# Kernel optimization log

Measured on AMD Instinct MI355X. Metric: run time of the kernel, lower is better.

The kernel has to match this reference:

```python
import jax, jax.numpy as jnp
import numpy as np

N_WIRES = 12
N_QLAYERS = 2
DIM = 2 ** N_WIRES


def setup_inputs() -> dict:
    key = jax.random.key(0)
    k0, k1, k2, k3 = jax.random.split(key, 4)
    x = jax.random.normal(k0, (2048, 1024), dtype=jnp.float32)
    # TT cores: ranks [1,16,1], input dims [32,32], output dims [8,9]
    core0 = jax.random.normal(k1, (1, 32, 8, 16), dtype=jnp.float32) * 0.05
    core1 = jax.random.normal(k2, (16, 32, 9, 1), dtype=jnp.float32) * 0.05
    tt_bias = jnp.zeros((72,), dtype=jnp.float32)
    global_angles = jax.random.normal(k3, (N_QLAYERS, N_WIRES, 3), dtype=jnp.float32) * 0.1
    return {"x": x, "core0": core0, "core1": core1, "tt_bias": tt_bias,
            "global_angles": global_angles}


def _rot(angles):
    # angles [..., 3] -> combined U = Rz @ Ry @ Rx, shape [..., 2, 2] complex64
    half = angles * 0.5
    cx, sx = jnp.cos(half[..., 0]), jnp.sin(half[..., 0])
    cy, sy = jnp.cos(half[..., 1]), jnp.sin(half[..., 1])
    cz, sz = jnp.cos(half[..., 2]), jnp.sin(half[..., 2])
    zero = jnp.zeros_like(cx)
    cplx = jax.lax.complex
    Rx = jnp.stack([jnp.stack([cplx(cx, zero), cplx(zero, -sx)], -1),
                    jnp.stack([cplx(zero, -sx), cplx(cx, zero)], -1)], -2)
    Ry = jnp.stack([jnp.stack([cplx(cy, zero), cplx(-sy, zero)], -1),
                    jnp.stack([cplx(sy, zero), cplx(cy, zero)], -1)], -2)
    ez, ezc = cplx(cz, -sz), cplx(cz, sz)  # exp(-i z/2), exp(+i z/2)
    zc = cplx(zero, zero)
    Rz = jnp.stack([jnp.stack([ez, zc], -1), jnp.stack([zc, ezc], -1)], -2)
    return jnp.einsum('...ij,...jk,...kl->...il', Rz, Ry, Rx)


def _apply_1q(state, U, w):
    # state [bsz, 2^n]; U [bsz, 2, 2]; wire 0 = most significant qubit
    bsz = state.shape[0]
    left, right = 2 ** w, 2 ** (N_WIRES - w - 1)
    s = state.reshape(bsz, left, 2, right)
    s = jnp.einsum('bij,bljr->blir', U, s)
    return s.reshape(bsz, DIM)


def _cnot(state, c, t):
    bsz = state.shape[0]
    s = state.reshape((bsz,) + (2,) * N_WIRES)
    s0 = jax.lax.index_in_dim(s, 0, c + 1, keepdims=True)
    s1 = jax.lax.index_in_dim(s, 1, c + 1, keepdims=True)
    s1 = jnp.flip(s1, axis=t + 1)  # flip target amplitudes where control = 1
    return jnp.concatenate([s0, s1], axis=c + 1).reshape(bsz, DIM)


def reference(x, core0, core1, tt_bias, global_angles):
    bsz = x.shape[0]
    # --- TT layer: x[b,32,32] contracted with two TT cores -> [b,8,9] -> [b,72]
    x_rs = x.reshape(bsz, 32, 32)
    tt_out = jnp.einsum('bij,aipq,qjrs->bpr', x_rs, core0, core1).reshape(bsz, -1) + tt_bias
    # residual global angles
    angles = global_angles[None, :, :, :] + tt_out.reshape(bsz, N_QLAYERS, N_WIRES, 3)
    U = _rot(angles)  # [bsz, L, n, 2, 2]
    # --- tensor-product Ry encoding of x[:, :n_wires] on |0...0>
    enc = x[:, :N_WIRES] * 0.5
    amp = jnp.stack([jnp.cos(enc), jnp.sin(enc)], -1)  # [bsz, n, 2]
    state = amp[:, 0, :]
    for w in range(1, N_WIRES):
        state = (state[:, :, None] * amp[:, w, None, :]).reshape(bsz, -1)
    state = state.astype(jnp.complex64)  # [bsz, 2^n]
    # --- VQC layers: fused Rz@Ry@Rx per wire, then ring CNOT (noise_prob=0)
    for k in range(N_QLAYERS):
        for w in range(N_WIRES):
            state = _apply_1q(state, U[:, k, w], w)
        for i in range(N_WIRES - 1):
            state = _cnot(state, i, i + 1)
        state = _cnot(state, N_WIRES - 1, 0)
    # --- MeasureAll(PauliZ): <Z_w> per wire
    probs = jnp.real(state * jnp.conj(state))  # [bsz, 2^n]
    idx = jnp.arange(DIM)[:, None]
    bits = (idx >> jnp.arange(N_WIRES - 1, -1, -1)[None, :]) & 1  # [2^n, n]
    zsign = (1.0 - 2.0 * bits).astype(jnp.float32)
    return probs @ zsign  # [bsz, n_wires]
```

## Files before the change

### kernel.cpp

```cpp
#include <hip/hip_runtime.h>
#include <math.h>

#define N_WIRES 12

__host__ __device__ constexpr int parity12(int x) {
  x ^= x >> 8; x ^= x >> 4; x ^= x >> 2; x ^= x >> 1;
  return x & 1;
}

__host__ __device__ constexpr int lanemask_of(int m) {
  return (((m >> 9) & 1) << 0) | (((m >> 8) & 1) << 1) |
         (((m >> 11) & 1) << 2) | (((m >> 10) & 1) << 3) |
         (((m >> 7) & 1) << 4) | (((m >> 6) & 1) << 5);
}

typedef float2 f2;
__device__ __forceinline__ f2 mk2(float a, float b) { f2 r; r.x = a; r.y = b; return r; }
__device__ __forceinline__ f2 pkmul(f2 a, f2 b) {
  f2 d; asm("v_pk_mul_f32 %0, %1, %2" : "=v"(d) : "v"(a), "v"(b)); return d;
}
__device__ __forceinline__ f2 pkfma(f2 a, f2 b, f2 c) {
  f2 d; asm("v_pk_fma_f32 %0, %1, %2, %3" : "=v"(d) : "v"(a), "v"(b), "v"(c)); return d;
}
__device__ __forceinline__ f2 swap2(f2 v) { return mk2(v.y, v.x); }

struct cpx { float r, i; };
__device__ __forceinline__ cpx cmulc(cpx a, cpx b) {
  return {a.r * b.r - a.i * b.i, a.r * b.i + a.i * b.r};
}
__device__ __forceinline__ cpx fpick(float r0, float i0, float r1, float i1, int b) {
  cpx c; c.r = b ? r1 : r0; c.i = b ? i1 : i0; return c;
}
__device__ __forceinline__ float rl(float v, int l) {
  return __int_as_float(__builtin_amdgcn_readlane(__float_as_int(v), l));
}

template <int LM>
__device__ __forceinline__ float lshfl(float v, int lane) {
  if constexpr (LM == 0) {
    return v;
  } else if constexpr (LM == 0x01) {
    return __int_as_float(__builtin_amdgcn_mov_dpp(__float_as_int(v), 0xB1, 0xF, 0xF, true));
  } else if constexpr (LM == 0x02) {
    return __int_as_float(__builtin_amdgcn_mov_dpp(__float_as_int(v), 0x4E, 0xF, 0xF, true));
  } else if constexpr (LM == 0x03) {
    return __int_as_float(__builtin_amdgcn_mov_dpp(__float_as_int(v), 0x1B, 0xF, 0xF, true));
  } else if constexpr ((LM & 0x20) != 0) {
#if __has_builtin(__builtin_amdgcn_permlane32_swap)
    auto p = __builtin_amdgcn_permlane32_swap(__float_as_int(v), __float_as_int(v), false, false);
    const float tv = __int_as_float((lane & 32) ? (int)p[0] : (int)p[1]);
    return lshfl<LM & 0x1F>(tv, lane);
#else
    return __shfl_xor(v, LM, 64);
#endif
  } else if constexpr (LM == 0x10) {
#if __has_builtin(__builtin_amdgcn_permlane16_swap)
    auto p = __builtin_amdgcn_permlane16_swap(__float_as_int(v), __float_as_int(v), false, false);
    return __int_as_float((lane & 16) ? (int)p[0] : (int)p[1]);
#else
    return __int_as_float(__builtin_amdgcn_ds_swizzle(__float_as_int(v), (0x10 << 10) | 0x1F));
#endif
  } else {
    return __int_as_float(__builtin_amdgcn_ds_swizzle(__float_as_int(v), (LM << 10) | 0x1F));
  }
}
template <int LM>
__device__ __forceinline__ f2 lshfl2(f2 v, int lane) {
  return mk2(lshfl<LM>(v.x, lane), lshfl<LM>(v.y, lane));
}

__global__ __launch_bounds__(256) void build_w_kernel(
    const float* __restrict__ core0,
    const float* __restrict__ core1,
    float* __restrict__ Wt) {
  int idx = blockIdx.x * 256 + threadIdx.x;
  int k = idx / 72;
  int o = idx - k * 72;
  int i = k >> 5, jj = k & 31;
  int p = o / 9, r = o - p * 9;
  float acc = 0.f;
#pragma unroll
  for (int q = 0; q < 16; ++q) {
    acc += core0[(i * 8 + p) * 16 + q] * core1[(q * 32 + jj) * 9 + r];
  }
  int og = o / 9, j = o - og * 9;
  Wt[k * 96 + og * 12 + j] = acc;
}

__global__ __launch_bounds__(512) void tt_gemm3(
    const float* __restrict__ x,
    const float* __restrict__ Wt,
    const float* __restrict__ bias,
    float* __restrict__ ttout) {
  __shared__ __align__(16) float xs[8 * 132];
  __shared__ float part[16 * 8 * 73];
  const int t = threadIdx.x;
  const int row0 = blockIdx.x * 8;
  const int kk = t >> 5;
  const int rp = (t >> 3) & 3;
  const int og = t & 7;
  const int r0 = rp * 2;

  float a0[9], a1[9];
#pragma unroll
  for (int j = 0; j < 9; ++j) { a0[j] = 0.f; a1[j] = 0.f; }

  for (int s = 0; s < 8; ++s) {
    __syncthreads();
    if (t < 256) {
      const int rr = t >> 5, j4 = t & 31;
      *(float4*)&xs[rr * 132 + j4 * 4] =
          *(const float4*)(x + (size_t)(row0 + rr) * 1024 + s * 128 + j4 * 4);
    }
    __syncthreads();
    const float* Wp = Wt + (size_t)s * 128 * 96;
#pragma unroll
    for (int i = 0; i < 8; ++i) {
      const int k = kk + i * 16;
      const float4 wA = *(const float4*)(Wp + k * 96 + og * 12);
      const float4 wB = *(const float4*)(Wp + k * 96 + og * 12 + 4);
      const float w8 = Wp[k * 96 + og * 12 + 8];
      const float x0v = xs[r0 * 132 + k];
      const float x1v = xs[r0 * 132 + 132 + k];
      a0[0] += x0v * wA.x; a0[1] += x0v * wA.y;
      a0[2] += x0v * wA.z; a0[3] += x0v * wA.w;
      a0[4] += x0v * wB.x; a0[5] += x0v * wB.y;
      a0[6] += x0v * wB.z; a0[7] += x0v * wB.w;
      a0[8] += x0v * w8;
      a1[0] += x1v * wA.x; a1[1] += x1v * wA.y;
      a1[2] += x1v * wA.z; a1[3] += x1v * wA.w;
      a1[4] += x1v * wB.x; a1[5] += x1v * wB.y;
      a1[6] += x1v * wB.z; a1[7] += x1v * wB.w;
      a1[8] += x1v * w8;
    }
  }

#pragma unroll
  for (int j = 0; j < 9; ++j) {
    part[(kk * 8 + r0) * 73 + og * 9 + j] = a0[j];
    part[(kk * 8 + r0 + 1) * 73 + og * 9 + j] = a1[j];
  }
  __syncthreads();

  for (int i = t; i < 576; i += 512) {
    const int r = i / 72, o = i - r * 72;
    float ssum = bias[o];
#pragma unroll
    for (int kq = 0; kq < 16; ++kq) ssum += part[(kq * 8 + r) * 73 + o];
    ttout[(size_t)(row0 + r) * 72 + o] = ssum;
  }
}

template <int MASK, int ROW>
__device__ __forceinline__ void gate_pk(f2 R[32], f2 I[32],
    float u00r, float u00i, float u01r, float u01i, int lane) {
  constexpr int RM = MASK & 0x3F;
  constexpr int LMP = lanemask_of(MASK);
  constexpr int ROWL = lanemask_of(ROW);
  constexpr int FLIP = parity12(ROW & 3);
  constexpr int JX = (RM == 0) ? 0 : (((RM & 1) ? (RM ^ 3) : RM) >> 1);
  constexpr bool SW = (RM & 1) != 0;

  const int tsgn = (__popc(ROWL & lane) & 1) << 31;
  const float dEi = __int_as_float(__float_as_int(u00i) ^ tsgn);
  const float oEr = __int_as_float(__float_as_int(u01r) ^ tsgn);
  const float ndEi = -dEi, noEr = -oEr;
  const f2 A  = mk2(u00r, u00r);
  const f2 C  = mk2(u01i, u01i);
  const f2 nC = mk2(-u01i, -u01i);

  auto Dof = [&](int pe, int ph) { return mk2(pe ? ndEi : dEi, ph ? ndEi : dEi); };
  auto Oof = [&](int pe, int ph) { return mk2(pe ? noEr : oEr, ph ? noEr : oEr); };

  auto upd = [&](int j, f2 Rb, f2 Ib, f2& outR, f2& outI) {
    const int pe = parity12(ROW & (2 * j));
    const int ph = pe ^ FLIP;
    const f2 Dj = Dof(pe, ph), nDj = Dof(!pe, !ph), Oj = Oof(pe, ph);
    const f2 a = R[j], ii = I[j];
    outR = pkfma(A, a, pkfma(nDj, ii, pkfma(Oj, Rb, pkmul(nC, Ib))));
    outI = pkfma(Dj, a, pkfma(A, ii, pkfma(C, Rb, pkmul(Oj, Ib))));
  };

  if constexpr (LMP != 0 && RM == 0) {
#pragma unroll
    for (int j = 0; j < 32; ++j) {
      const f2 Rb = lshfl2<LMP>(R[j], lane);
      const f2 Ib = lshfl2<LMP>(I[j], lane);
      f2 nR, nI;
      upd(j, Rb, Ib, nR, nI);
      R[j] = nR; I[j] = nI;
    }
  } else if constexpr (LMP != 0 && RM != 0) {
#pragma unroll
    for (int j = 0; j < 32; ++j) {
      const int j2 = j ^ JX;
      if (j < j2) {
        f2 Rb1 = lshfl2<LMP>(R[j2], lane), Ib1 = lshfl2<LMP>(I[j2], lane);
        f2 Rb2 = lshfl2<LMP>(R[j],  lane), Ib2 = lshfl2<LMP>(I[j],  lane);
        if constexpr (SW) {
          Rb1 = swap2(Rb1); Ib1 = swap2(Ib1);
          Rb2 = swap2(Rb2); Ib2 = swap2(Ib2);
        }
        f2 nR1, nI1, nR2, nI2;
        upd(j, Rb1, Ib1, nR1, nI1);
        upd(j2, Rb2, Ib2, nR2, nI2);
        R[j] = nR1; I[j] = nI1; R[j2] = nR2; I[j2] = nI2;
      }
    }
  } else {
#pragma unroll
    for (int j = 0; j < 32; ++j) {
      const int j2 = j ^ JX;
      if (j < j2) {
        f2 Rb1 = R[j2], Ib1 = I[j2], Rb2 = R[j], Ib2 = I[j];
        if constexpr (SW) {
          Rb1 = swap2(Rb1); Ib1 = swap2(Ib1);
          Rb2 = swap2(Rb2); Ib2 = swap2(Ib2);
        }
        f2 nR1, nI1, nR2, nI2;
        upd(j, Rb1, Ib1, nR1, nI1);
        upd(j2, Rb2, Ib2, nR2, nI2);
        R[j] = nR1; I[j] = nI1; R[j2] = nR2; I[j2] = nI2;
      }
    }
  }
}

__global__ __launch_bounds__(256, 2) void vqc_kernel7(
    const float* __restrict__ x,
    const float* __restrict__ ttout,
    const float* __restrict__ gang,
    float* __restrict__ out) {
  const int t = threadIdx.x;
  const int lane = t & 63;
  const int b = blockIdx.x * 4 + (t >> 6);
  const float* ttb = ttout + (size_t)b * 72;

  float c0 = 0.f, c1 = 0.f, c2 = 0.f, c3 = 0.f;
  const bool uLane = lane < 12;
  const bool fLane = (lane >= 16) && (lane < 28);
  if (uLane || fLane) {
    const int w = uLane ? lane : lane - 16;
    const int k = uLane ? 1 : 0;
    const int gbase = (k * 12 + w) * 3;
    const int tbase = k * 36 + w * 3;
    const float a0 = gang[gbase + 0] + ttb[tbase + 0];
    const float a1 = gang[gbase + 1] + ttb[tbase + 1];
    const float a2 = gang[gbase + 2] + ttb[tbase + 2];
    const float cx = cosf(0.5f * a0), sx = sinf(0.5f * a0);
    const float cy = cosf(0.5f * a1), sy = sinf(0.5f * a1);
    const float cz = cosf(0.5f * a2), sz = sinf(0.5f * a2);
    const float m00r = cy * cx,   m00i = sy * sx;
    const float m01r = -sy * cx,  m01i = -cy * sx;
    const float m10r = sy * cx,   m10i = -cy * sx;
    const float m11r = cy * cx,   m11i = -sy * sx;
    const float U00r = cz * m00r + sz * m00i, U00i = cz * m00i - sz * m00r;
    const float U01r = cz * m01r + sz * m01i, U01i = cz * m01i - sz * m01r;
    const float U10r = cz * m10r - sz * m10i, U10i = cz * m10i + sz * m10r;
    const float U11r = cz * m11r - sz * m11i, U11i = cz * m11i + sz * m11r;
    if (uLane) {
      c0 = U00r; c1 = U00i; c2 = U01r; c3 = U01i;
    } else {
      const float e = x[(size_t)b * 1024 + w] * 0.5f;
      const float cc = cosf(e), ss = sinf(e);
      c0 = U00r * cc + U01r * ss;  c1 = U00i * cc + U01i * ss;
      c2 = U10r * cc + U11r * ss;  c3 = U10i * cc + U11i * ss;
    }
  }

  const int bwv0 = (lane >> 2) & 1;
  const int bwv1 = ((lane >> 3) ^ lane) & 1;
  const int bwv2 = (lane ^ (lane >> 1)) & 1;
  const int bwv3 = ((lane >> 1) ^ (lane >> 4)) & 1;
  const int bwv4 = ((lane >> 4) ^ (lane >> 5)) & 1;
  const int l5 = (lane >> 5) & 1;

  cpx P = fpick(rl(c0, 16), rl(c1, 16), rl(c2, 16), rl(c3, 16), bwv0);
  P = cmulc(P, fpick(rl(c0, 17), rl(c1, 17), rl(c2, 17), rl(c3, 17), bwv1));
  P = cmulc(P, fpick(rl(c0, 18), rl(c1, 18), rl(c2, 18), rl(c3, 18), bwv2));
  P = cmulc(P, fpick(rl(c0, 19), rl(c1, 19), rl(c2, 19), rl(c3, 19), bwv3));
  P = cmulc(P, fpick(rl(c0, 20), rl(c1, 20), rl(c2, 20), rl(c3, 20), bwv4));

  cpx PT[8];
  {
    const cpx F5a = fpick(rl(c0, 21), rl(c1, 21), rl(c2, 21), rl(c3, 21), l5);
    const cpx F5b = fpick(rl(c0, 21), rl(c1, 21), rl(c2, 21), rl(c3, 21), l5 ^ 1);
    cpx F6[2], F7[2];
    F6[0] = {rl(c0, 22), rl(c1, 22)};  F6[1] = {rl(c2, 22), rl(c3, 22)};
    F7[0] = {rl(c0, 23), rl(c1, 23)};  F7[1] = {rl(c2, 23), rl(c3, 23)};
    const cpx P5a = cmulc(P, F5a), P5b = cmulc(P, F5b);
    cpx t56[4];
#pragma unroll
    for (int i = 0; i < 4; ++i) {
      const int r5 = i >> 1, r4 = i & 1;
      t56[i] = cmulc(r5 ? P5b : P5a, F6[r5 ^ r4]);
    }
#pragma unroll
    for (int i = 0; i < 8; ++i) {
      const int r4 = (i >> 1) & 1, r3 = i & 1;
      PT[i] = cmulc(t56[i >> 1], F7[r4 ^ r3]);
    }
  }

  cpx TL[16];
  {
    cpx F8[2], F9[2], F10[2], F11[2];
    F8[0]  = {rl(c0, 24), rl(c1, 24)};  F8[1]  = {rl(c2, 24), rl(c3, 24)};
    F9[0]  = {rl(c0, 25), rl(c1, 25)};  F9[1]  = {rl(c2, 25), rl(c3, 25)};
    F10[0] = {rl(c0, 26), rl(c1, 26)};  F10[1] = {rl(c2, 26), rl(c3, 26)};
    F11[0] = {rl(c0, 27), rl(c1, 27)};  F11[1] = {rl(c2, 27), rl(c3, 27)};
    cpx t10[4];
#pragma unroll
    for (int i = 0; i < 4; ++i) {
      const int r1 = i >> 1, r0 = i & 1;
      t10[i] = cmulc(F10[r1 ^ r0], F11[r0]);
    }
    cpx t9[8];
#pragma unroll
    for (int i = 0; i < 8; ++i) {
      const int r2 = i >> 2, r1 = (i >> 1) & 1;
      t9[i] = cmulc(F9[r2 ^ r1], t10[i & 3]);
    }
#pragma unroll
    for (int i = 0; i < 16; ++i) {
      const int r3 = i >> 3, r2 = (i >> 2) & 1;
      TL[i] = cmulc(F8[r3 ^ r2], t9[i & 7]);
    }
  }

  f2 R[32], I[32];
#pragma unroll
  for (int j = 0; j < 32; ++j) {
    const cpx Av = PT[(j >> 2) & 7];
    const int il = (2 * j) & 15;
    const f2 Tre = mk2(TL[il].r, TL[il ^ 3].r);
    const f2 Tim = mk2(TL[il].i, TL[il ^ 3].i);
    const f2 Ar = mk2(Av.r, Av.r);
    R[j] = pkfma(mk2(-Av.i, -Av.i), Tim, pkmul(Ar, Tre));
    I[j] = pkfma(mk2(Av.i, Av.i), Tre, pkmul(Ar, Tim));
  }

#define GATE(MASK, ROW, G)                                                  \
  gate_pk<MASK, ROW>(R, I, rl(c0, G), rl(c1, G), rl(c2, G), rl(c3, G), lane)

  GATE(0xC00, 0x400, 0);
  GATE(0x200, 0xE00, 1);
  GATE(0x100, 0xD00, 2);
  GATE(0x080, 0xC80, 3);
  GATE(0x040, 0xC40, 4);
  GATE(0x020, 0xC20, 5);
  GATE(0x010, 0xC10, 6);
  GATE(0x008, 0xC08, 7);
  GATE(0x004, 0xC04, 8);
  GATE(0x002, 0xC02, 9);
  GATE(0x001, 0xC01, 10);
  GATE(0xBFF, 0xC00, 11);
#undef GATE

  constexpr int MROWS[12] = {0xFFF, 0xA00, 0x700, 0xB80, 0x7C0, 0xBE0,
                             0x7F0, 0xBF8, 0x7FC, 0xBFE, 0x7FF, 0xBFF};
  const f2 Spp = mk2(1.f, 1.f),  Smm = mk2(-1.f, -1.f);
  const f2 Spm = mk2(1.f, -1.f), Smp = mk2(-1.f, 1.f);
  f2 acc2[12];
#pragma unroll
  for (int w = 0; w < 12; ++w) acc2[w] = mk2(0.f, 0.f);
#pragma unroll
  for (int j = 0; j < 32; ++j) {
    const f2 pr2 = pkfma(I[j], I[j], pkmul(R[j], R[j]));
#pragma unroll
    for (int w = 0; w < 12; ++w) {
      const int sl = parity12(MROWS[w] & (2 * j));
      const int sh = sl ^ parity12(MROWS[w] & 3);
      const f2 S = sl ? (sh ? Smm : Smp) : (sh ? Spm : Spp);
      acc2[w] = pkfma(S, pr2, acc2[w]);
    }
  }
#pragma unroll
  for (int w = 0; w < 12; ++w) {
    float v = acc2[w].x + acc2[w].y;
    if (__popc(lanemask_of(MROWS[w]) & lane) & 1) v = -v;
#pragma unroll
    for (int off = 32; off > 0; off >>= 1) v += __shfl_down(v, off, 64);
    if (lane == 0) out[(size_t)b * 12 + w] = v;
  }
}

extern "C" void kernel_launch(void* const* d_in, const int* in_sizes, int n_in,
                              void* d_out, int out_size, void* d_ws, size_t ws_size,
                              hipStream_t stream) {
  const float* x       = (const float*)d_in[0];
  const float* core0   = (const float*)d_in[1];
  const float* core1   = (const float*)d_in[2];
  const float* tt_bias = (const float*)d_in[3];
  const float* gang    = (const float*)d_in[4];
  float* out = (float*)d_out;
  float* Wt     = (float*)d_ws;
  float* ttout  = (float*)d_ws + 98304;

  const int bsz = in_sizes[0] / 1024;

  build_w_kernel<<<288, 256, 0, stream>>>(core0, core1, Wt);
  tt_gemm3<<<bsz / 8, 512, 0, stream>>>(x, Wt, tt_bias, ttout);
  vqc_kernel7<<<bsz / 4, 256, 0, stream>>>(x, ttout, gang, out);
}
```

Measured before the change: 57.07 us.

## Split each VQC state across two waves and stage W tiles in LDS

Each 4096-amplitude state vector is now split across two wavefronts, 16 register pairs per lane instead of 32. The most-significant qubit lives on the wave index, and its gate exchanges amplitudes through shared memory behind block barriers. Lane shuffles move to DPP row-mirror variants, with a final cross-wave reduction done in LDS. The TT GEMM also stages each W tile in shared memory instead of reading it from global memory per thread. This raises occupancy and lowers register pressure, at the cost of barriers, LDS traffic and a larger shared-memory footprint.

Result: faster. 50.34 us (-11.8%).

```diff
diff --git a/kernel.cpp b/kernel.cpp
--- a/kernel.cpp
+++ b/kernel.cpp
@@ -10,8 +10,8 @@
 
 __host__ __device__ constexpr int lanemask_of(int m) {
   return (((m >> 9) & 1) << 0) | (((m >> 8) & 1) << 1) |
-         (((m >> 11) & 1) << 2) | (((m >> 10) & 1) << 3) |
-         (((m >> 7) & 1) << 4) | (((m >> 6) & 1) << 5);
+         (((m >> 7) & 1) << 2) | (((m >> 6) & 1) << 3) |
+         (((m >> 5) & 1) << 4) | (((m >> 11) & 1) << 5);
 }
 
 typedef float2 f2;
@@ -35,38 +35,39 @@
   return __int_as_float(__builtin_amdgcn_readlane(__float_as_int(v), l));
 }
 
+template <int CTRL>
+__device__ __forceinline__ float dppmov(float v) {
+  return __int_as_float(
+      __builtin_amdgcn_mov_dpp(__float_as_int(v), CTRL, 0xF, 0xF, true));
+}
+
 template <int LM>
-__device__ __forceinline__ float lshfl(float v, int lane) {
+__device__ __forceinline__ float lshfl(float v) {
   if constexpr (LM == 0) {
     return v;
   } else if constexpr (LM == 0x01) {
-    return __int_as_float(__builtin_amdgcn_mov_dpp(__float_as_int(v), 0xB1, 0xF, 0xF, true));
+    return dppmov<0xB1>(v);
   } else if constexpr (LM == 0x02) {
-    return __int_as_float(__builtin_amdgcn_mov_dpp(__float_as_int(v), 0x4E, 0xF, 0xF, true));
+    return dppmov<0x4E>(v);
   } else if constexpr (LM == 0x03) {
-    return __int_as_float(__builtin_amdgcn_mov_dpp(__float_as_int(v), 0x1B, 0xF, 0xF, true));
-  } else if constexpr ((LM & 0x20) != 0) {
-#if __has_builtin(__builtin_amdgcn_permlane32_swap)
-    auto p = __builtin_amdgcn_permlane32_swap(__float_as_int(v), __float_as_int(v), false, false);
-    const float tv = __int_as_float((lane & 32) ? (int)p[0] : (int)p[1]);
-    return lshfl<LM & 0x1F>(tv, lane);
-#else
+    return dppmov<0x1B>(v);
+  } else if constexpr (LM == 0x04) {
+    return dppmov<0x1B>(dppmov<0x141>(v));
+  } else if constexpr (LM == 0x07) {
+    return dppmov<0x141>(v);
+  } else if constexpr (LM == 0x08) {
+    return dppmov<0x141>(dppmov<0x140>(v));
+  } else if constexpr (LM == 0x0F) {
+    return dppmov<0x140>(v);
+  } else if constexpr ((LM & 0x30) != 0) {
+    return lshfl<LM & 0x0F>(__shfl_xor(v, LM & 0x30, 64));
+  } else {
     return __shfl_xor(v, LM, 64);
-#endif
-  } else if constexpr (LM == 0x10) {
-#if __has_builtin(__builtin_amdgcn_permlane16_swap)
-    auto p = __builtin_amdgcn_permlane16_swap(__float_as_int(v), __float_as_int(v), false, false);
-    return __int_as_float((lane & 16) ? (int)p[0] : (int)p[1]);
-#else
-    return __int_as_float(__builtin_amdgcn_ds_swizzle(__float_as_int(v), (0x10 << 10) | 0x1F));
-#endif
-  } else {
-    return __int_as_float(__builtin_amdgcn_ds_swizzle(__float_as_int(v), (LM << 10) | 0x1F));
   }
 }
 template <int LM>
-__device__ __forceinline__ f2 lshfl2(f2 v, int lane) {
-  return mk2(lshfl<LM>(v.x, lane), lshfl<LM>(v.y, lane));
+__device__ __forceinline__ f2 lshfl2(f2 v) {
+  return mk2(lshfl<LM>(v.x), lshfl<LM>(v.y));
 }
 
 __global__ __launch_bounds__(256) void build_w_kernel(
@@ -87,11 +88,12 @@
   Wt[k * 96 + og * 12 + j] = acc;
 }
 
-__global__ __launch_bounds__(512) void tt_gemm3(
+__global__ __launch_bounds__(512) void tt_gemm2(
     const float* __restrict__ x,
     const float* __restrict__ Wt,
     const float* __restrict__ bias,
     float* __restrict__ ttout) {
+  __shared__ __align__(16) float ws[128 * 96];
   __shared__ __align__(16) float xs[8 * 132];
   __shared__ float part[16 * 8 * 73];
   const int t = threadIdx.x;
@@ -107,19 +109,24 @@
 
   for (int s = 0; s < 8; ++s) {
     __syncthreads();
+    const float4* Wg = (const float4*)(Wt + s * 128 * 96);
+#pragma unroll
+    for (int i = 0; i < 6; ++i) {
+      const int idx = i * 512 + t;
+      ((float4*)ws)[idx] = Wg[idx];
+    }
     if (t < 256) {
       const int rr = t >> 5, j4 = t & 31;
       *(float4*)&xs[rr * 132 + j4 * 4] =
           *(const float4*)(x + (size_t)(row0 + rr) * 1024 + s * 128 + j4 * 4);
     }
     __syncthreads();
-    const float* Wp = Wt + (size_t)s * 128 * 96;
 #pragma unroll
     for (int i = 0; i < 8; ++i) {
       const int k = kk + i * 16;
-      const float4 wA = *(const float4*)(Wp + k * 96 + og * 12);
-      const float4 wB = *(const float4*)(Wp + k * 96 + og * 12 + 4);
-      const float w8 = Wp[k * 96 + og * 12 + 8];
+      const float4 wA = *(const float4*)&ws[k * 96 + og * 12];
+      const float4 wB = *(const float4*)&ws[k * 96 + og * 12 + 4];
+      const float w8 = ws[k * 96 + og * 12 + 8];
       const float x0v = xs[r0 * 132 + k];
       const float x1v = xs[r0 * 132 + 132 + k];
       a0[0] += x0v * wA.x; a0[1] += x0v * wA.y;
@@ -152,16 +159,19 @@
 }
 
 template <int MASK, int ROW>
-__device__ __forceinline__ void gate_pk(f2 R[32], f2 I[32],
-    float u00r, float u00i, float u01r, float u01i, int lane) {
-  constexpr int RM = MASK & 0x3F;
-  constexpr int LMP = lanemask_of(MASK);
+__device__ __forceinline__ void gate9(f2 R[16], f2 I[16],
+    float u00r, float u00i, float u01r, float u01i,
+    f2* __restrict__ buf, int t, int lane, int wq) {
+  constexpr int RM   = MASK & 0x1F;
+  constexpr int LMP  = lanemask_of(MASK);
+  constexpr int WB   = (MASK >> 10) & 1;
   constexpr int ROWL = lanemask_of(ROW);
+  constexpr int RWB  = (ROW >> 10) & 1;
   constexpr int FLIP = parity12(ROW & 3);
   constexpr int JX = (RM == 0) ? 0 : (((RM & 1) ? (RM ^ 3) : RM) >> 1);
   constexpr bool SW = (RM & 1) != 0;
 
-  const int tsgn = (__popc(ROWL & lane) & 1) << 31;
+  const int tsgn = ((__popc(ROWL & lane) ^ (RWB & wq)) & 1) << 31;
   const float dEi = __int_as_float(__float_as_int(u00i) ^ tsgn);
   const float oEr = __int_as_float(__float_as_int(u01r) ^ tsgn);
   const float ndEi = -dEi, noEr = -oEr;
@@ -181,22 +191,41 @@
     outI = pkfma(Dj, a, pkfma(A, ii, pkfma(C, Rb, pkmul(Oj, Ib))));
   };
 
-  if constexpr (LMP != 0 && RM == 0) {
-#pragma unroll
-    for (int j = 0; j < 32; ++j) {
-      const f2 Rb = lshfl2<LMP>(R[j], lane);
-      const f2 Ib = lshfl2<LMP>(I[j], lane);
+  if constexpr (WB) {
+    static_assert(RM == 0, "wave-crossing gate must have no reg part");
+    const int tp = t ^ 64 ^ LMP;
+#pragma unroll
+    for (int ph2 = 0; ph2 < 2; ++ph2) {
+      __syncthreads();
+#pragma unroll
+      for (int j = 0; j < 8; ++j) {
+        buf[(j * 2 + 0) * 256 + t] = R[ph2 * 8 + j];
+        buf[(j * 2 + 1) * 256 + t] = I[ph2 * 8 + j];
+      }
+      __syncthreads();
+#pragma unroll
+      for (int j = 0; j < 8; ++j) {
+        const f2 Rb = buf[(j * 2 + 0) * 256 + tp];
+        const f2 Ib = buf[(j * 2 + 1) * 256 + tp];
+        upd(ph2 * 8 + j, Rb, Ib, R[ph2 * 8 + j], I[ph2 * 8 + j]);
+      }
+    }
+  } else if constexpr (LMP != 0 && RM == 0) {
+#pragma unroll
+    for (int j = 0; j < 16; ++j) {
+      const f2 Rb = lshfl2<LMP>(R[j]);
+      const f2 Ib = lshfl2<LMP>(I[j]);
       f2 nR, nI;
       upd(j, Rb, Ib, nR, nI);
       R[j] = nR; I[j] = nI;
     }
   } else if constexpr (LMP != 0 && RM != 0) {
 #pragma unroll
-    for (int j = 0; j < 32; ++j) {
+    for (int j = 0; j < 16; ++j) {
       const int j2 = j ^ JX;
       if (j < j2) {
-        f2 Rb1 = lshfl2<LMP>(R[j2], lane), Ib1 = lshfl2<LMP>(I[j2], lane);
-        f2 Rb2 = lshfl2<LMP>(R[j],  lane), Ib2 = lshfl2<LMP>(I[j],  lane);
+        f2 Rb1 = lshfl2<LMP>(R[j2]), Ib1 = lshfl2<LMP>(I[j2]);
+        f2 Rb2 = lshfl2<LMP>(R[j]),  Ib2 = lshfl2<LMP>(I[j]);
         if constexpr (SW) {
           Rb1 = swap2(Rb1); Ib1 = swap2(Ib1);
           Rb2 = swap2(Rb2); Ib2 = swap2(Ib2);
@@ -209,7 +238,7 @@
     }
   } else {
 #pragma unroll
-    for (int j = 0; j < 32; ++j) {
+    for (int j = 0; j < 16; ++j) {
       const int j2 = j ^ JX;
       if (j < j2) {
         f2 Rb1 = R[j2], Ib1 = I[j2], Rb2 = R[j], Ib2 = I[j];
@@ -226,15 +255,19 @@
   }
 }
 
-__global__ __launch_bounds__(256, 2) void vqc_kernel7(
+__global__ __launch_bounds__(256, 3) void vqc_kernel9(
     const float* __restrict__ x,
     const float* __restrict__ ttout,
     const float* __restrict__ gang,
     float* __restrict__ out) {
   const int t = threadIdx.x;
   const int lane = t & 63;
-  const int b = blockIdx.x * 4 + (t >> 6);
+  const int wq = (t >> 6) & 1;
+  const int row = t >> 7;
+  const int b = blockIdx.x * 2 + row;
   const float* ttb = ttout + (size_t)b * 72;
+
+  __shared__ __align__(16) f2 buf[4096];
 
   float c0 = 0.f, c1 = 0.f, c2 = 0.f, c3 = 0.f;
   const bool uLane = lane < 12;
@@ -268,80 +301,76 @@
     }
   }
 
-  const int bwv0 = (lane >> 2) & 1;
-  const int bwv1 = ((lane >> 3) ^ lane) & 1;
-  const int bwv2 = (lane ^ (lane >> 1)) & 1;
-  const int bwv3 = ((lane >> 1) ^ (lane >> 4)) & 1;
-  const int bwv4 = ((lane >> 4) ^ (lane >> 5)) & 1;
-  const int l5 = (lane >> 5) & 1;
-
-  cpx P = fpick(rl(c0, 16), rl(c1, 16), rl(c2, 16), rl(c3, 16), bwv0);
-  P = cmulc(P, fpick(rl(c0, 17), rl(c1, 17), rl(c2, 17), rl(c3, 17), bwv1));
-  P = cmulc(P, fpick(rl(c0, 18), rl(c1, 18), rl(c2, 18), rl(c3, 18), bwv2));
-  P = cmulc(P, fpick(rl(c0, 19), rl(c1, 19), rl(c2, 19), rl(c3, 19), bwv3));
-  P = cmulc(P, fpick(rl(c0, 20), rl(c1, 20), rl(c2, 20), rl(c3, 20), bwv4));
+  const int bw0 = (lane >> 5) & 1;
+  const int bw1 = (wq ^ lane) & 1;
+  const int bw2 = (lane ^ (lane >> 1)) & 1;
+  const int bw3 = ((lane >> 1) ^ (lane >> 2)) & 1;
+  const int bw4 = ((lane >> 2) ^ (lane >> 3)) & 1;
+  const int bw5 = ((lane >> 3) ^ (lane >> 4)) & 1;
+  const int l4 = (lane >> 4) & 1;
+
+  cpx P = fpick(rl(c0, 16), rl(c1, 16), rl(c2, 16), rl(c3, 16), bw0);
+  P = cmulc(P, fpick(rl(c0, 17), rl(c1, 17), rl(c2, 17), rl(c3, 17), bw1));
+  P = cmulc(P, fpick(rl(c0, 18), rl(c1, 18), rl(c2, 18), rl(c3, 18), bw2));
+  P = cmulc(P, fpick(rl(c0, 19), rl(c1, 19), rl(c2, 19), rl(c3, 19), bw3));
+  P = cmulc(P, fpick(rl(c0, 20), rl(c1, 20), rl(c2, 20), rl(c3, 20), bw4));
+  P = cmulc(P, fpick(rl(c0, 21), rl(c1, 21), rl(c2, 21), rl(c3, 21), bw5));
 
   cpx PT[8];
   {
-    const cpx F5a = fpick(rl(c0, 21), rl(c1, 21), rl(c2, 21), rl(c3, 21), l5);
-    const cpx F5b = fpick(rl(c0, 21), rl(c1, 21), rl(c2, 21), rl(c3, 21), l5 ^ 1);
-    cpx F6[2], F7[2];
-    F6[0] = {rl(c0, 22), rl(c1, 22)};  F6[1] = {rl(c2, 22), rl(c3, 22)};
+    const cpx F6a = fpick(rl(c0, 22), rl(c1, 22), rl(c2, 22), rl(c3, 22), l4);
+    const cpx F6b = fpick(rl(c0, 22), rl(c1, 22), rl(c2, 22), rl(c3, 22), l4 ^ 1);
+    cpx F7[2], F8[2];
     F7[0] = {rl(c0, 23), rl(c1, 23)};  F7[1] = {rl(c2, 23), rl(c3, 23)};
-    const cpx P5a = cmulc(P, F5a), P5b = cmulc(P, F5b);
-    cpx t56[4];
+    F8[0] = {rl(c0, 24), rl(c1, 24)};  F8[1] = {rl(c2, 24), rl(c3, 24)};
+    const cpx P6a = cmulc(P, F6a), P6b = cmulc(P, F6b);
+    cpx t67[4];
 #pragma unroll
     for (int i = 0; i < 4; ++i) {
-      const int r5 = i >> 1, r4 = i & 1;
-      t56[i] = cmulc(r5 ? P5b : P5a, F6[r5 ^ r4]);
+      const int r4 = i >> 1, r3 = i & 1;
+      t67[i] = cmulc(r4 ? P6b : P6a, F7[r4 ^ r3]);
     }
 #pragma unroll
     for (int i = 0; i < 8; ++i) {
-      const int r4 = (i >> 1) & 1, r3 = i & 1;
-      PT[i] = cmulc(t56[i >> 1], F7[r4 ^ r3]);
-    }
-  }
-
-  cpx TL[16];
+      const int r3 = (i >> 1) & 1, r2 = i & 1;
+      PT[i] = cmulc(t67[i >> 1], F8[r3 ^ r2]);
+    }
+  }
+
+  cpx TLo[8];
   {
-    cpx F8[2], F9[2], F10[2], F11[2];
-    F8[0]  = {rl(c0, 24), rl(c1, 24)};  F8[1]  = {rl(c2, 24), rl(c3, 24)};
+    cpx F9[2], F10[2], F11[2];
     F9[0]  = {rl(c0, 25), rl(c1, 25)};  F9[1]  = {rl(c2, 25), rl(c3, 25)};
     F10[0] = {rl(c0, 26), rl(c1, 26)};  F10[1] = {rl(c2, 26), rl(c3, 26)};
     F11[0] = {rl(c0, 27), rl(c1, 27)};  F11[1] = {rl(c2, 27), rl(c3, 27)};
-    cpx t10[4];
+    cpx t01[4];
 #pragma unroll
     for (int i = 0; i < 4; ++i) {
       const int r1 = i >> 1, r0 = i & 1;
-      t10[i] = cmulc(F10[r1 ^ r0], F11[r0]);
-    }
-    cpx t9[8];
+      t01[i] = cmulc(F10[r1 ^ r0], F11[r0]);
+    }
 #pragma unroll
     for (int i = 0; i < 8; ++i) {
       const int r2 = i >> 2, r1 = (i >> 1) & 1;
-      t9[i] = cmulc(F9[r2 ^ r1], t10[i & 3]);
-    }
-#pragma unroll
-    for (int i = 0; i < 16; ++i) {
-      const int r3 = i >> 3, r2 = (i >> 2) & 1;
-      TL[i] = cmulc(F8[r3 ^ r2], t9[i & 7]);
-    }
-  }
-
-  f2 R[32], I[32];
-#pragma unroll
-  for (int j = 0; j < 32; ++j) {
-    const cpx Av = PT[(j >> 2) & 7];
-    const int il = (2 * j) & 15;
-    const f2 Tre = mk2(TL[il].r, TL[il ^ 3].r);
-    const f2 Tim = mk2(TL[il].i, TL[il ^ 3].i);
+      TLo[i] = cmulc(F9[r2 ^ r1], t01[i & 3]);
+    }
+  }
+
+  f2 R[16], I[16];
+#pragma unroll
+  for (int j = 0; j < 16; ++j) {
+    const cpx Av = PT[j >> 1];
+    const int il = (2 * j) & 7;
+    const f2 Tre = mk2(TLo[il].r, TLo[il ^ 3].r);
+    const f2 Tim = mk2(TLo[il].i, TLo[il ^ 3].i);
     const f2 Ar = mk2(Av.r, Av.r);
     R[j] = pkfma(mk2(-Av.i, -Av.i), Tim, pkmul(Ar, Tre));
     I[j] = pkfma(mk2(Av.i, Av.i), Tre, pkmul(Ar, Tim));
   }
 
 #define GATE(MASK, ROW, G)                                                  \
-  gate_pk<MASK, ROW>(R, I, rl(c0, G), rl(c1, G), rl(c2, G), rl(c3, G), lane)
+  gate9<MASK, ROW>(R, I, rl(c0, G), rl(c1, G), rl(c2, G), rl(c3, G),        \
+                   buf, t, lane, wq)
 
   GATE(0xC00, 0x400, 0);
   GATE(0x200, 0xE00, 1);
@@ -365,7 +394,7 @@
 #pragma unroll
   for (int w = 0; w < 12; ++w) acc2[w] = mk2(0.f, 0.f);
 #pragma unroll
-  for (int j = 0; j < 32; ++j) {
+  for (int j = 0; j < 16; ++j) {
     const f2 pr2 = pkfma(I[j], I[j], pkmul(R[j], R[j]));
 #pragma unroll
     for (int w = 0; w < 12; ++w) {
@@ -375,13 +404,23 @@
       acc2[w] = pkfma(S, pr2, acc2[w]);
     }
   }
+  __syncthreads();
+  float* sred = (float*)buf;
 #pragma unroll
   for (int w = 0; w < 12; ++w) {
     float v = acc2[w].x + acc2[w].y;
-    if (__popc(lanemask_of(MROWS[w]) & lane) & 1) v = -v;
+    const int sg = (__popc(lanemask_of(MROWS[w]) & lane) ^
+                    (wq & ((MROWS[w] >> 10) & 1))) & 1;
+    if (sg) v = -v;
 #pragma unroll
     for (int off = 32; off > 0; off >>= 1) v += __shfl_down(v, off, 64);
-    if (lane == 0) out[(size_t)b * 12 + w] = v;
+    if (lane == 0) sred[(t >> 6) * 12 + w] = v;
+  }
+  __syncthreads();
+  if (t < 24) {
+    const int rr = t / 12, w = t - rr * 12;
+    out[(size_t)(blockIdx.x * 2 + rr) * 12 + w] =
+        sred[(rr * 2) * 12 + w] + sred[(rr * 2 + 1) * 12 + w];
   }
 }
 
@@ -400,6 +439,6 @@
   const int bsz = in_sizes[0] / 1024;
 
   build_w_kernel<<<288, 256, 0, stream>>>(core0, core1, Wt);
-  tt_gemm3<<<bsz / 8, 512, 0, stream>>>(x, Wt, tt_bias, ttout);
-  vqc_kernel7<<<bsz / 4, 256, 0, stream>>>(x, ttout, gang, out);
-}
+  tt_gemm2<<<bsz / 8, 512, 0, stream>>>(x, Wt, tt_bias, ttout);
+  vqc_kernel9<<<bsz / 2, 256, 0, stream>>>(x, ttout, gang, out);
+}
```
